# Optimization experiments

Measured on AMD Instinct MI355X. Metric: run time of the kernel, lower is better.

Reference implementation:

```python
import jax, jax.numpy as jnp
import numpy as np

N, E, G = 50000, 800000, 128
IN, HID, HEAD = 1280, 256, 4
DH = HID // HEAD
EPS = 1e-5
ATT_SCALE = 1.0 / np.sqrt(1280.0).astype(np.float32)  # hardcoded in source


def _seg_softmax(x, seg, n):
    # softmax over segments along axis 0; x: [K] or [K, H]
    m = jax.ops.segment_max(x, seg, num_segments=n)
    e = jnp.exp(x - m[seg])
    s = jax.ops.segment_sum(e, seg, num_segments=n)
    return e / s[seg]


def _bn(x, g, b):
    # eval-mode BatchNorm1d with init running stats (mean=0, var=1)
    return g * x * (1.0 / np.sqrt(1.0 + EPS)) + b


def _ln(x, g, b):
    mu = x.mean(-1, keepdims=True)
    var = ((x - mu) ** 2).mean(-1, keepdims=True)
    return g * (x - mu) / jnp.sqrt(var + EPS) + b


def setup_inputs() -> dict:
    key = jax.random.key(0)
    ks = jax.random.split(key, 40)
    rn = lambda i, shp, s=0.05: jax.random.normal(ks[i], shp, jnp.float32) * s
    inp = {
        "h": jax.random.normal(ks[0], (N, IN), jnp.float32),
        "gcn_w0": rn(1, (IN, HID)), "gcn_b0": rn(2, (HID,), 0.01),
        "gcn_w1": rn(3, (HID, HID)), "gcn_b1": rn(4, (HID,), 0.01),
        "bn_gcn0_g": 1.0 + rn(5, (HID,), 0.1), "bn_gcn0_b": rn(6, (HID,), 0.01),
        "bn_gcn1_g": 1.0 + rn(7, (HID,), 0.1), "bn_gcn1_b": rn(8, (HID,), 0.01),
        "gat_w0": rn(9, (IN, HID)), "gat_al0": rn(10, (HEAD, DH)), "gat_ar0": rn(11, (HEAD, DH)), "gat_bias0": rn(12, (HID,), 0.01),
        "gat_w1": rn(13, (HID, HID)), "gat_al1": rn(14, (HEAD, DH)), "gat_ar1": rn(15, (HEAD, DH)), "gat_bias1": rn(16, (HID,), 0.01),
        "bn_gat0_g": 1.0 + rn(17, (HID,), 0.1), "bn_gat0_b": rn(18, (HID,), 0.01),
        "bn_gat1_g": 1.0 + rn(19, (HID,), 0.1), "bn_gat1_b": rn(20, (HID,), 0.01),
        "gate_w": rn(21, (2 * HID, HID)), "gate_b": rn(22, (HID,), 0.01),
        "qw": rn(23, (HEAD, HID, HID)), "kw": rn(24, (HEAD, HID, HID)), "vw": rn(25, (HEAD, HID, HID)),
        "ct_w": rn(26, (HEAD * HID, HID)),
        "ff_w1": rn(27, (HID, 2 * HID)), "ff_b1": rn(28, (2 * HID,), 0.01),
        "ff_w2": rn(29, (2 * HID, HID)), "ff_b2": rn(30, (HID,), 0.01),
        "ln_g": 1.0 + rn(31, (HID,), 0.1), "ln_b": rn(32, (HID,), 0.01),
        "src": jax.random.randint(ks[33], (E,), 0, N, jnp.int32),
        "dst": jax.random.randint(ks[34], (E,), 0, N, jnp.int32),
        "gid": jnp.sort(jax.random.randint(ks[35], (N,), 0, G, jnp.int32)),
        "num_graphs": G,
    }
    return inp


def reference(h, gcn_w0, gcn_b0, gcn_w1, gcn_b1, bn_gcn0_g, bn_gcn0_b, bn_gcn1_g, bn_gcn1_b,
              gat_w0, gat_al0, gat_ar0, gat_bias0, gat_w1, gat_al1, gat_ar1, gat_bias1,
              bn_gat0_g, bn_gat0_b, bn_gat1_g, bn_gat1_b, gate_w, gate_b,
              qw, kw, vw, ct_w, ff_w1, ff_b1, ff_w2, ff_b2, ln_g, ln_b,
              src, dst, gid, num_graphs):
    n = h.shape[0]
    ones_e = jnp.ones(src.shape[0], h.dtype)
    # dgl.mean_nodes per graph
    cnt = jnp.clip(jax.ops.segment_sum(jnp.ones(n, h.dtype), gid, num_segments=num_graphs), 1.0)
    init_avg_h = jax.ops.segment_sum(h, gid, num_segments=num_graphs) / cnt[:, None]
    # GraphConv norm='both', degrees clamped to >=1
    deg_out = jnp.clip(jax.ops.segment_sum(ones_e, src, num_segments=n), 1.0)
    deg_in = jnp.clip(jax.ops.segment_sum(ones_e, dst, num_segments=n), 1.0)
    ns, nd = deg_out ** -0.5, deg_in ** -0.5

    def gcn(x, w, b):
        m = (x * ns[:, None]) @ w  # [N, HID]
        return jax.ops.segment_sum(m[src], dst, num_segments=n) * nd[:, None] + b

    hg = jax.nn.relu(_bn(gcn(h, gcn_w0, gcn_b0), bn_gcn0_g, bn_gcn0_b))
    hg = jax.nn.relu(_bn(gcn(hg, gcn_w1, gcn_b1), bn_gcn1_g, bn_gcn1_b)) + hg

    def gat(x, w, al, ar, b):
        f = (x @ w).reshape(n, HEAD, DH)
        el = (f * al).sum(-1)  # [N, HEAD]
        er = (f * ar).sum(-1)
        e = jax.nn.leaky_relu(el[src] + er[dst], 0.2)  # [E, HEAD]
        alpha = _seg_softmax(e, dst, n)  # edge softmax over incoming edges
        out = jax.ops.segment_sum(alpha[:, :, None] * f[src], dst, num_segments=n)
        return out.reshape(n, HID) + b

    ha = jax.nn.elu(_bn(gat(h, gat_w0, gat_al0, gat_ar0, gat_bias0), bn_gat0_g, bn_gat0_b))
    ha = jax.nn.elu(_bn(gat(ha, gat_w1, gat_al1, gat_ar1, gat_bias1), bn_gat1_g, bn_gat1_b)) + ha

    gate = jax.nn.sigmoid(jnp.concatenate([hg, ha], axis=1) @ gate_w + gate_b)
    x = gate * hg + (1.0 - gate) * ha  # residue_h

    # transformer_block: per-graph node softmax attention
    q = jnp.einsum('nd,hde->nhe', x, qw)
    k = jnp.einsum('nd,hde->nhe', x, kw)
    v = jnp.einsum('nd,hde->nhe', x, vw)
    att = (q * k).sum(-1) * ATT_SCALE  # [N, HEAD]
    alpha = _seg_softmax(att, gid, num_graphs)  # dgl.softmax_nodes per head
    mo = (v * alpha[:, :, None]).reshape(n, HEAD * HID) @ ct_w
    x1 = _ln(mo + x, ln_g, ln_b)
    x2 = _ln(jax.nn.relu(x1 @ ff_w1 + ff_b1) @ ff_w2 + ff_b2 + x1, ln_g, ln_b)

    readout = jax.ops.segment_sum(x2, gid, num_segments=num_graphs)
    return readout, init_avg_h
```

## Files before the change

### kernel.cpp

```cpp
#include <hip/hip_runtime.h>

#define NN 50000
#define NE 800000
#define NG 128
#define DIN 1280
#define HIDDEN 256
#define BNS 0.9999950000374997f
#define ATT_SCALE 0.027950849718747373f
#define LN_EPS 1e-5f

typedef __attribute__((ext_vector_type(8))) short short8;
typedef __attribute__((ext_vector_type(4))) float floatx4;

__device__ __forceinline__ float b2f(unsigned short u) {
  return __uint_as_float(((unsigned int)u) << 16);
}
__device__ __forceinline__ unsigned short f2b(float f) {
  unsigned int x = __float_as_uint(f);
  x += 0x7fffu + ((x >> 16) & 1u);
  return (unsigned short)(x >> 16);
}

__device__ __forceinline__ void tr_dev(const float* __restrict__ src,
                                       unsigned short* __restrict__ dst,
                                       int K, int Nc, int bi) {
  int idx = bi * 256 + threadIdx.x;
  if (idx >= K * Nc) return;
  int n = idx / K, k = idx % K;
  dst[idx] = f2b(src[(size_t)k * Nc + n]);
}

__global__ void prep_all_k(const float* __restrict__ gcn_w0, const float* __restrict__ gat_w0,
                           const float* __restrict__ gcn_w1, const float* __restrict__ gat_w1,
                           const float* __restrict__ gate_w, const float* __restrict__ ff_w1,
                           const float* __restrict__ ff_w2, const float* __restrict__ qw,
                           const float* __restrict__ kw, const float* __restrict__ vw,
                           const float* __restrict__ ctw,
                           unsigned short* __restrict__ w01t, unsigned short* __restrict__ w1t,
                           unsigned short* __restrict__ w1gt, unsigned short* __restrict__ gatewt,
                           unsigned short* __restrict__ ffw1t, unsigned short* __restrict__ ffw2t,
                           unsigned short* __restrict__ wmvt, unsigned short* __restrict__ w2t) {
  int b = blockIdx.x;
  if (b < 1280) { tr_dev(gcn_w0, w01t, 1280, 256, b); return; }
  if (b < 2560) { tr_dev(gat_w0, w01t + 256 * 1280, 1280, 256, b - 1280); return; }
  if (b < 2816) { tr_dev(gcn_w1, w1t, 256, 256, b - 2560); return; }
  if (b < 3072) { tr_dev(gat_w1, w1gt, 256, 256, b - 2816); return; }
  if (b < 3584) { tr_dev(gate_w, gatewt, 512, 256, b - 3072); return; }
  if (b < 4096) { tr_dev(ff_w1, ffw1t, 256, 512, b - 3584); return; }
  if (b < 4608) { tr_dev(ff_w2, ffw2t, 512, 256, b - 4096); return; }
  if (b < 5632) {
    int col = b - 4608;
    int d = threadIdx.x;
    int hh = col >> 8, dp = col & 255;
    const float* qr = qw + ((size_t)hh * 256 + d) * 256;
    const float* kr = kw + ((size_t)hh * 256 + dp) * 256;
    float s = 0.f;
    for (int e = 0; e < 256; e += 4) {
      float4 a = *(const float4*)(qr + e);
      float4 bb = *(const float4*)(kr + e);
      s += a.x * bb.x + a.y * bb.y + a.z * bb.z + a.w * bb.w;
    }
    wmvt[(size_t)col * 256 + d] = f2b(s);
    return;
  }
  {
    int bb = b - 5632;
    int c = threadIdx.x;
    int hh = bb >> 8, d = bb & 255;
    const float* vr = vw + ((size_t)hh * 256 + d) * 256;
    float s = 0.f;
    for (int e = 0; e < 256; ++e)
      s += vr[e] * ctw[(size_t)(hh * 256 + e) * 256 + c];
    w2t[(size_t)c * 1024 + bb] = f2b(s);
  }
}

__global__ void cvt_avg_k(const float* __restrict__ h, const int* __restrict__ gid,
                          unsigned short* __restrict__ h_bf, float* __restrict__ out1) {
  int row0 = blockIdx.x * 50;
  int tid = threadIdx.x;
  float4 acc = {0.f, 0.f, 0.f, 0.f};
  int cur_g = gid[row0];
  int c4 = tid * 4;
  for (int r = 0; r < 50; ++r) {
    int row = row0 + r;
    int g = gid[row];
    if (g != cur_g) {
      atomicAdd(&out1[(size_t)cur_g * DIN + c4 + 0], acc.x);
      atomicAdd(&out1[(size_t)cur_g * DIN + c4 + 1], acc.y);
      atomicAdd(&out1[(size_t)cur_g * DIN + c4 + 2], acc.z);
      atomicAdd(&out1[(size_t)cur_g * DIN + c4 + 3], acc.w);
      acc = {0.f, 0.f, 0.f, 0.f};
      cur_g = g;
    }
    float4 v = *(const float4*)(h + (size_t)row * DIN + c4);
    acc.x += v.x; acc.y += v.y; acc.z += v.z; acc.w += v.w;
    ushort4 o;
    o.x = f2b(v.x); o.y = f2b(v.y); o.z = f2b(v.z); o.w = f2b(v.w);
    *(ushort4*)(h_bf + (size_t)row * DIN + c4) = o;
  }
  atomicAdd(&out1[(size_t)cur_g * DIN + c4 + 0], acc.x);
  atomicAdd(&out1[(size_t)cur_g * DIN + c4 + 1], acc.y);
  atomicAdd(&out1[(size_t)cur_g * DIN + c4 + 2], acc.z);
  atomicAdd(&out1[(size_t)cur_g * DIN + c4 + 3], acc.w);
}

__global__ void div_avg_k(const int* __restrict__ start, float* __restrict__ out1) {
  int idx = blockIdx.x * 256 + threadIdx.x;
  if (idx >= NG * DIN) return;
  int g = idx / DIN;
  float cnt = (float)(start[g + 1] - start[g]);
  if (cnt < 1.f) cnt = 1.f;
  out1[idx] /= cnt;
}

__global__ void bounds_deg_k(const int* __restrict__ gid, int* __restrict__ start,
                             const int* __restrict__ src, const int* __restrict__ dst,
                             int* __restrict__ deg_out, int* __restrict__ deg_in) {
  int i = blockIdx.x * 256 + threadIdx.x;
  if (i < NN) {
    int g = gid[i];
    if (i == 0) {
      for (int gg = 0; gg <= g; ++gg) start[gg] = 0;
    } else {
      int gp = gid[i - 1];
      for (int gg = gp + 1; gg <= g; ++gg) start[gg] = i;
    }
    if (i == NN - 1) {
      for (int gg = g + 1; gg <= NG; ++gg) start[gg] = NN;
    }
  }
  if (i < NE) {
    atomicAdd(&deg_out[src[i]], 1);
    atomicAdd(&deg_in[dst[i]], 1);
  }
}

__global__ void scan_local_k(const int* __restrict__ deg_in, const int* __restrict__ deg_out,
                             int* __restrict__ row_ptr, int* __restrict__ bsum,
                             float* __restrict__ ns, float* __restrict__ nd) {
  __shared__ int buf[256];
  int b = blockIdx.x, t = threadIdx.x;
  int i = b * 256 + t;
  int v = (i < NN) ? deg_in[i] : 0;
  buf[t] = v;
  __syncthreads();
  for (int off = 1; off < 256; off <<= 1) {
    int tv = (t >= off) ? buf[t - off] : 0;
    __syncthreads();
    buf[t] += tv;
    __syncthreads();
  }
  if (i < NN) {
    row_ptr[i] = buf[t] - v;
    int a = deg_out[i]; if (a < 1) a = 1;
    int bb = v;         if (bb < 1) bb = 1;
    ns[i] = rsqrtf((float)a);
    nd[i] = rsqrtf((float)bb);
  }
  if (t == 255) bsum[b] = buf[255];
}

__global__ void scan_bsum_k(int* __restrict__ bsum, int* __restrict__ boff, int nb,
                            int* __restrict__ row_ptr) {
  __shared__ int buf[256];
  int t = threadIdx.x;
  int v = (t < nb) ? bsum[t] : 0;
  buf[t] = v;
  __syncthreads();
  for (int off = 1; off < 256; off <<= 1) {
    int tv = (t >= off) ? buf[t - off] : 0;
    __syncthreads();
    buf[t] += tv;
    __syncthreads();
  }
  if (t < nb) boff[t] = buf[t] - v;
  if (t == 0) row_ptr[NN] = NE;
}

__global__ void scan_add_k(int* __restrict__ row_ptr, const int* __restrict__ boff) {
  int i = blockIdx.x * 256 + threadIdx.x;
  if (i >= NN) return;
  row_ptr[i] += boff[blockIdx.x];
}

__global__ void fill_csr_k(const int* __restrict__ src, const int* __restrict__ dst,
                           const int* __restrict__ row_ptr, int* __restrict__ fill,
                           int* __restrict__ csr_src, int e) {
  int i = blockIdx.x * 256 + threadIdx.x;
  if (i >= e) return;
  int d = dst[i];
  int pos = row_ptr[d] + atomicAdd(&fill[d], 1);
  csr_src[pos] = src[i];
}

template <int MODE>
__global__ __launch_bounds__(256, 2) void gemm_bf16(const unsigned short* __restrict__ A,
                                                    const unsigned short* __restrict__ Bt,
                                                    void* __restrict__ Cout,
                                                    const float* __restrict__ bias,
                                                    int M, int K, int Nc,
                                                    const unsigned short* __restrict__ xtile,
                                                    float* __restrict__ attp,
                                                    const float* __restrict__ ascale,
                                                    const float* __restrict__ al,
                                                    const float* __restrict__ ar,
                                                    float* __restrict__ elr,
                                                    int ecol0) {
  __shared__ unsigned short sbuf[32768];
  const int tid = threadIdx.x;
  const int n0 = blockIdx.x * 128;
  const int m0 = blockIdx.y * 128;
  const int w = tid >> 6;
  const int lane = tid & 63;
  const int wr = (w >> 1) * 64;
  const int wc = (w & 1) * 64;
  const int quad = lane >> 4;
  const int l15 = lane & 15;
  const int js = tid & 7;
  const int mbase = tid >> 3;
  const int wbase = w * 64;

  bool do_elr = (MODE == 8);
  const unsigned short* Ap = A;
  const unsigned short* Bp = Bt;
  unsigned short* Cp = (unsigned short*)Cout;
  if (MODE == 8 && gridDim.z == 2) {
    if (blockIdx.z == 0) {
      do_elr = false;
    } else {
      Ap += 12800000;
      Bp += 65536;
      Cp += 12800000;
    }
  }

  floatx4 acc[4][4];
#pragma unroll
  for (int i = 0; i < 4; ++i)
#pragma unroll
    for (int j = 0; j < 4; ++j) acc[i][j] = (floatx4)0.0f;

  if constexpr (MODE == 6) {
    unsigned short* lA = sbuf;
    unsigned short* lB = sbuf + 8192;
    for (int k0 = 0; k0 < K; k0 += 64) {
      __syncthreads();
#pragma unroll
      for (int it = 0; it < 4; ++it) {
        int m = it * 32 + mbase;
        int gm = m0 + m;
        if (gm >= M) gm = M - 1;
        uint4 va = *(const uint4*)(Ap + (size_t)gm * 256 + (k0 & 255) + js * 8);
        float s = ascale[(size_t)gm * 4 + (k0 >> 8)];
        unsigned short* pp = (unsigned short*)&va;
#pragma unroll
        for (int c = 0; c < 8; ++c) pp[c] = f2b(b2f(pp[c]) * s);
        *(uint4*)(lA + (size_t)(m * 8 + (js ^ (m & 7))) * 8) = va;
      }
#pragma unroll
      for (int it = 0; it < 4; ++it) {
        int c = it * 256 + wbase + lane;
        int m = c >> 3, g = c & 7;
        int gn = n0 + m;
        const unsigned short* gp = Bp + (size_t)gn * K + k0 + (g ^ (m & 7)) * 8;
        __builtin_amdgcn_global_load_lds(
            (const __attribute__((address_space(1))) unsigned int*)gp,
            (__attribute__((address_space(3))) unsigned int*)(lB + (size_t)(it * 256 + wbase) * 8),
            16, 0, 0);
      }
      __syncthreads();
#pragma unroll
      for (int ks = 0; ks < 2; ++ks) {
        int kb = ks * 4 + quad;
        short8 af[4], bfr[4];
#pragma unroll
        for (int ri = 0; ri < 4; ++ri) {
          int r = wr + ri * 16 + l15;
          af[ri] = *(const short8*)(lA + (size_t)(r * 8 + (kb ^ (r & 7))) * 8);
        }
#pragma unroll
        for (int ci = 0; ci < 4; ++ci) {
          int c = wc + ci * 16 + l15;
          bfr[ci] = *(const short8*)(lB + (size_t)(c * 8 + (kb ^ (c & 7))) * 8);
        }
#pragma unroll
        for (int ri = 0; ri < 4; ++ri)
#pragma unroll
          for (int ci = 0; ci < 4; ++ci)
            acc[ri][ci] = __builtin_amdgcn_mfma_f32_16x16x32_bf16(af[ri], bfr[ci], acc[ri][ci], 0, 0, 0);
      }
    }
    __syncthreads();
  } else {
    const int nt = K >> 6;
    auto stage = [&](int b, int k0) {
      unsigned short* lA = sbuf + b * 16384;
      unsigned short* lB = lA + 8192;
#pragma unroll
      for (int it = 0; it < 4; ++it) {
        int c = it * 256 + wbase + lane;
        int m = c >> 3, g = c & 7;
        int gm = m0 + m;
        if (gm >= M) gm = M - 1;
        const unsigned short* gp = Ap + (size_t)gm * K + k0 + (g ^ (m & 7)) * 8;
        __builtin_amdgcn_global_load_lds(
            (const __attribute__((address_space(1))) unsigned int*)gp,
            (__attribute__((address_space(3))) unsigned int*)(lA + (size_t)(it * 256 + wbase) * 8),
            16, 0, 0);
      }
#pragma unroll
      for (int it = 0; it < 4; ++it) {
        int c = it * 256 + wbase + lane;
        int m = c >> 3, g = c & 7;
        int gn = n0 + m;
        const unsigned short* gp = Bp + (size_t)gn * K + k0 + (g ^ (m & 7)) * 8;
        __builtin_amdgcn_global_load_lds(
            (const __attribute__((address_space(1))) unsigned int*)gp,
            (__attribute__((address_space(3))) unsigned int*)(lB + (size_t)(it * 256 + wbase) * 8),
            16, 0, 0);
      }
    };
    stage(0, 0);
    __syncthreads();
    for (int t = 0; t < nt; ++t) {
      int cur = t & 1;
      if (t + 1 < nt) stage(cur ^ 1, (t + 1) * 64);
      unsigned short* lA = sbuf + cur * 16384;
      unsigned short* lB = lA + 8192;
#pragma unroll
      for (int ks = 0; ks < 2; ++ks) {
        int kb = ks * 4 + quad;
        short8 af[4], bfr[4];
#pragma unroll
        for (int ri = 0; ri < 4; ++ri) {
          int r = wr + ri * 16 + l15;
          af[ri] = *(const short8*)(lA + (size_t)(r * 8 + (kb ^ (r & 7))) * 8);
        }
#pragma unroll
        for (int ci = 0; ci < 4; ++ci) {
          int c = wc + ci * 16 + l15;
          bfr[ci] = *(const short8*)(lB + (size_t)(c * 8 + (kb ^ (c & 7))) * 8);
        }
#pragma unroll
        for (int ri = 0; ri < 4; ++ri)
#pragma unroll
          for (int ci = 0; ci < 4; ++ci)
            acc[ri][ci] = __builtin_amdgcn_mfma_f32_16x16x32_bf16(af[ri], bfr[ci], acc[ri][ci], 0, 0, 0);
      }
      __syncthreads();
    }
  }

  if (MODE == 4) {
    int cb = n0 & 255;
#pragma unroll
    for (int it2 = 0; it2 < 8; ++it2) {
      int linear = it2 * 256 + tid;
      int rr = linear >> 4;
      int c8 = (linear & 15) * 8;
      int gr = m0 + rr;
      if (gr >= M) gr = M - 1;
      *(uint4*)(sbuf + rr * 128 + c8) = *(const uint4*)(xtile + (size_t)gr * 256 + cb + c8);
    }
    __syncthreads();
    int head = n0 >> 8;
#pragma unroll
    for (int ri = 0; ri < 4; ++ri) {
      int lrow = wr + ri * 16 + quad * 4;
#pragma unroll
      for (int r = 0; r < 4; ++r) {
        float p = 0.f;
#pragma unroll
        for (int ci = 0; ci < 4; ++ci)
          p += acc[ri][ci][r] * b2f(sbuf[(lrow + r) * 128 + wc + ci * 16 + l15]);
        p += __shfl_xor(p, 1);
        p += __shfl_xor(p, 2);
        p += __shfl_xor(p, 4);
        p += __shfl_xor(p, 8);
        if (l15 == 0) {
          int grow = m0 + lrow + r;
          if (grow < M) atomicAdd(&attp[(size_t)grow * 4 + head], p * ATT_SCALE);
        }
      }
    }
    return;
  }

  if (MODE == 7) {
#pragma unroll
    for (int ri = 0; ri < 4; ++ri) {
      int row = m0 + wr + ri * 16 + quad * 4;
#pragma unroll
      for (int ci = 0; ci < 4; ++ci) {
        int col = n0 + wc + ci * 16 + l15;
        float bv = bias[col];
#pragma unroll
        for (int r = 0; r < 4; ++r) {
          if (row + r < M) {
            float g = 1.f / (1.f + expf(-(acc[ri][ci][r] + bv)));
            float hg = b2f(xtile[(size_t)(row + r) * 512 + col]);
            float ha = b2f(xtile[(size_t)(row + r) * 512 + 256 + col]);
            Cp[(size_t)(row + r) * Nc + col] = f2b(g * hg + (1.f - g) * ha);
          }
        }
      }
    }
    return;
  }

  if (MODE == 8 && do_elr && n0 >= ecol0) {
    int head = (n0 - ecol0 + wc) >> 6;
#pragma unroll
    for (int ri = 0; ri < 4; ++ri) {
      int lrow = wr + ri * 16 + quad * 4;
#pragma unroll
      for (int r = 0; r < 4; ++r) {
        float pl = 0.f, pr = 0.f;
#pragma unroll
        for (int ci = 0; ci < 4; ++ci) {
          float fv = acc[ri][ci][r];
          pl += fv * al[head * 64 + ci * 16 + l15];
          pr += fv * ar[head * 64 + ci * 16 + l15];
        }
        pl += __shfl_xor(pl, 1); pl += __shfl_xor(pl, 2);
        pl += __shfl_xor(pl, 4); pl += __shfl_xor(pl, 8);
        pr += __shfl_xor(pr, 1); pr += __shfl_xor(pr, 2);
        pr += __shfl_xor(pr, 4); pr += __shfl_xor(pr, 8);
        if (l15 == 0) {
          int grow = m0 + lrow + r;
          if (grow < M) {
            elr[(size_t)grow * 8 + head] = pl;
            elr[(size_t)grow * 8 + 4 + head] = pr;
          }
        }
      }
    }
  }

#pragma unroll
  for (int ri = 0; ri < 4; ++ri) {
    int row = m0 + wr + ri * 16 + quad * 4;
#pragma unroll
    for (int ci = 0; ci < 4; ++ci) {
      int col = n0 + wc + ci * 16 + l15;
      float bv = (MODE == 2) ? bias[col] : 0.f;
#pragma unroll
      for (int r = 0; r < 4; ++r) {
        if (row + r < M) {
          float v = acc[ri][ci][r];
          if (MODE == 2) { v += bv; v = fmaxf(v, 0.f); }
          if (MODE == 1)
            ((float*)Cout)[(size_t)(row + r) * Nc + col] = v;
          else
            Cp[(size_t)(row + r) * Nc + col] = f2b(v);
        }
      }
    }
  }
}

__global__ void gcn_agg_k(const unsigned short* __restrict__ m, int ldm,
                          const int* __restrict__ row_ptr, const int* __restrict__ csr_src,
                          const float* __restrict__ ns, const float* __restrict__ nd,
                          const float* __restrict__ bias,
                          const float* __restrict__ bng, const float* __restrict__ bnb,
                          const unsigned short* __restrict__ resid, int ldr,
                          unsigned short* __restrict__ out, int ldo) {
  int node = blockIdx.x * 4 + (threadIdx.x >> 6);
  if (node >= NN) return;
  int lane = threadIdx.x & 63;
  int s = row_ptr[node], e = row_ptr[node + 1];
  int eidx = lane & 15;
  float a0 = 0, a1 = 0, a2 = 0, a3 = 0;
  for (int i0 = s; i0 < e; i0 += 16) {
    int n16 = e - i0; if (n16 > 16) n16 = 16;
    int u_mine = 0; float w_mine = 0.f;
    if (eidx < n16) {
      u_mine = csr_src[i0 + eidx];
      w_mine = ns[u_mine];
    }
    for (int e2 = 0; e2 < n16; ++e2) {
      int sl = (lane & 48) | e2;
      int u = __shfl(u_mine, sl);
      float w = __shfl(w_mine, sl);
      ushort4 v = *(const ushort4*)(m + (size_t)u * ldm + lane * 4);
      a0 += w * b2f(v.x); a1 += w * b2f(v.y); a2 += w * b2f(v.z); a3 += w * b2f(v.w);
    }
  }
  float ndv = nd[node];
  int col = lane * 4;
  float vals[4] = {a0, a1, a2, a3};
  ushort4 o;
#pragma unroll
  for (int c = 0; c < 4; ++c) {
    float v = vals[c] * ndv + bias[col + c];
    v = bng[col + c] * v * BNS + bnb[col + c];
    v = fmaxf(v, 0.f);
    if (resid) v += b2f(resid[(size_t)node * ldr + col + c]);
    ((unsigned short*)&o)[c] = f2b(v);
  }
  *(ushort4*)(out + (size_t)node * ldo + col) = o;
}

__global__ void gat_agg_k(const unsigned short* __restrict__ f, int ldf,
                          const int* __restrict__ row_ptr, const int* __restrict__ csr_src,
                          const float* __restrict__ elr,
                          const float* __restrict__ bias,
                          const float* __restrict__ bng, const float* __restrict__ bnb,
                          const unsigned short* __restrict__ resid, int ldr,
                          unsigned short* __restrict__ out, int ldo) {
  int node = blockIdx.x * 4 + (threadIdx.x >> 6);
  if (node >= NN) return;
  int lane = threadIdx.x & 63;
  int s = row_ptr[node], e = row_ptr[node + 1];
  float4 er = *(const float4*)(elr + (size_t)node * 8 + 4);
  float m0 = -1e30f, m1 = -1e30f, m2 = -1e30f, m3 = -1e30f;
  for (int i = s + lane; i < e; i += 64) {
    int u = csr_src[i];
    float4 el = *(const float4*)(elr + (size_t)u * 8);
    float t;
    t = el.x + er.x; t = t > 0.f ? t : 0.2f * t; m0 = fmaxf(m0, t);
    t = el.y + er.y; t = t > 0.f ? t : 0.2f * t; m1 = fmaxf(m1, t);
    t = el.z + er.z; t = t > 0.f ? t : 0.2f * t; m2 = fmaxf(m2, t);
    t = el.w + er.w; t = t > 0.f ? t : 0.2f * t; m3 = fmaxf(m3, t);
  }
#pragma unroll
  for (int off = 1; off < 64; off <<= 1) {
    m0 = fmaxf(m0, __shfl_xor(m0, off));
    m1 = fmaxf(m1, __shfl_xor(m1, off));
    m2 = fmaxf(m2, __shfl_xor(m2, off));
    m3 = fmaxf(m3, __shfl_xor(m3, off));
  }
  float s0 = 0, s1 = 0, s2 = 0, s3 = 0;
  for (int i = s + lane; i < e; i += 64) {
    int u = csr_src[i];
    float4 el = *(const float4*)(elr + (size_t)u * 8);
    float t;
    t = el.x + er.x; t = t > 0.f ? t : 0.2f * t; s0 += expf(t - m0);
    t = el.y + er.y; t = t > 0.f ? t : 0.2f * t; s1 += expf(t - m1);
    t = el.z + er.z; t = t > 0.f ? t : 0.2f * t; s2 += expf(t - m2);
    t = el.w + er.w; t = t > 0.f ? t : 0.2f * t; s3 += expf(t - m3);
  }
#pragma unroll
  for (int off = 1; off < 64; off <<= 1) {
    s0 += __shfl_xor(s0, off);
    s1 += __shfl_xor(s1, off);
    s2 += __shfl_xor(s2, off);
    s3 += __shfl_xor(s3, off);
  }
  int head = lane >> 4;
  float erh = head == 0 ? er.x : head == 1 ? er.y : head == 2 ? er.z : er.w;
  float mh = head == 0 ? m0 : head == 1 ? m1 : head == 2 ? m2 : m3;
  float sh = head == 0 ? s0 : head == 1 ? s1 : head == 2 ? s2 : s3;
  float inv_sh = (sh > 0.f) ? 1.f / sh : 0.f;
  int eidx = lane & 15;
  float a0 = 0, a1 = 0, a2 = 0, a3 = 0;
  for (int i0 = s; i0 < e; i0 += 16) {
    int n16 = e - i0; if (n16 > 16) n16 = 16;
    int u_mine = 0; float w_mine = 0.f;
    if (eidx < n16) {
      u_mine = csr_src[i0 + eidx];
      float el = elr[(size_t)u_mine * 8 + head];
      float t = el + erh;
      t = t > 0.f ? t : 0.2f * t;
      w_mine = expf(t - mh) * inv_sh;
    }
    for (int e2 = 0; e2 < n16; ++e2) {
      int sl = (lane & 48) | e2;
      int u = __shfl(u_mine, sl);
      float wgt = __shfl(w_mine, sl);
      ushort4 v = *(const ushort4*)(f + (size_t)u * ldf + lane * 4);
      a0 += wgt * b2f(v.x); a1 += wgt * b2f(v.y); a2 += wgt * b2f(v.z); a3 += wgt * b2f(v.w);
    }
  }
  int col = lane * 4;
  float vals[4] = {a0, a1, a2, a3};
  ushort4 o;
#pragma unroll
  for (int c = 0; c < 4; ++c) {
    float v = vals[c] + bias[col + c];
    v = bng[col + c] * v * BNS + bnb[col + c];
    v = (v > 0.f) ? v : (expf(v) - 1.f);
    if (resid) v += b2f(resid[(size_t)node * ldr + col + c]);
    ((unsigned short*)&o)[c] = f2b(v);
  }
  *(ushort4*)(out + (size_t)node * ldo + col) = o;
}

__global__ void gsoftmax_k(const float* __restrict__ att, const int* __restrict__ start,
                           float* __restrict__ alpha) {
  int g = blockIdx.x;
  int s = start[g], e = start[g + 1];
  int tid = threadIdx.x;
  __shared__ float red[256];
  __shared__ float mh[4], sh[4];
  float lm[4] = {-1e30f, -1e30f, -1e30f, -1e30f};
  for (int i = s + tid; i < e; i += 256) {
    float4 a = *(const float4*)(att + (size_t)i * 4);
    lm[0] = fmaxf(lm[0], a.x); lm[1] = fmaxf(lm[1], a.y);
    lm[2] = fmaxf(lm[2], a.z); lm[3] = fmaxf(lm[3], a.w);
  }
#pragma unroll
  for (int h = 0; h < 4; ++h) {
    red[tid] = lm[h]; __syncthreads();
    for (int off = 128; off > 0; off >>= 1) {
      if (tid < off) red[tid] = fmaxf(red[tid], red[tid + off]);
      __syncthreads();
    }
    if (tid == 0) mh[h] = red[0];
    __syncthreads();
  }
  float ls[4] = {0, 0, 0, 0};
  for (int i = s + tid; i < e; i += 256) {
    float4 a = *(const float4*)(att + (size_t)i * 4);
    ls[0] += expf(a.x - mh[0]); ls[1] += expf(a.y - mh[1]);
    ls[2] += expf(a.z - mh[2]); ls[3] += expf(a.w - mh[3]);
  }
#pragma unroll
  for (int h = 0; h < 4; ++h) {
    red[tid] = ls[h]; __syncthreads();
    for (int off = 128; off > 0; off >>= 1) {
      if (tid < off) red[tid] += red[tid + off];
      __syncthreads();
    }
    if (tid == 0) sh[h] = red[0];
    __syncthreads();
  }
  for (int i = s + tid; i < e; i += 256) {
    float4 a = *(const float4*)(att + (size_t)i * 4);
    float4 o;
    o.x = expf(a.x - mh[0]) / sh[0];
    o.y = expf(a.y - mh[1]) / sh[1];
    o.z = expf(a.z - mh[2]) / sh[2];
    o.w = expf(a.w - mh[3]) / sh[3];
    *(float4*)(alpha + (size_t)i * 4) = o;
  }
}

__global__ void ln1_k(const unsigned short* __restrict__ mo, const unsigned short* __restrict__ x,
                      const float* __restrict__ g, const float* __restrict__ b,
                      unsigned short* __restrict__ x1) {
  int node = blockIdx.x * 4 + (threadIdx.x >> 6);
  if (node >= NN) return;
  int lane = threadIdx.x & 63;
  int c = lane * 4;
  ushort4 a = *(const ushort4*)(mo + (size_t)node * HIDDEN + c);
  ushort4 xx = *(const ushort4*)(x + (size_t)node * HIDDEN + c);
  float v0 = b2f(a.x) + b2f(xx.x), v1 = b2f(a.y) + b2f(xx.y);
  float v2 = b2f(a.z) + b2f(xx.z), v3 = b2f(a.w) + b2f(xx.w);
  float sm = v0 + v1 + v2 + v3;
#pragma unroll
  for (int off = 1; off < 64; off <<= 1) sm += __shfl_xor(sm, off);
  float mu = sm * (1.f / 256.f);
  float d0 = v0 - mu, d1 = v1 - mu, d2 = v2 - mu, d3 = v3 - mu;
  float sq = d0 * d0 + d1 * d1 + d2 * d2 + d3 * d3;
#pragma unroll
  for (int off = 1; off < 64; off <<= 1) sq += __shfl_xor(sq, off);
  float inv = rsqrtf(sq * (1.f / 256.f) + LN_EPS);
  ushort4 ob;
  ob.x = f2b(g[c + 0] * d0 * inv + b[c + 0]);
  ob.y = f2b(g[c + 1] * d1 * inv + b[c + 1]);
  ob.z = f2b(g[c + 2] * d2 * inv + b[c + 2]);
  ob.w = f2b(g[c + 3] * d3 * inv + b[c + 3]);
  *(ushort4*)(x1 + (size_t)node * HIDDEN + c) = ob;
}

__global__ void ln2_k(const unsigned short* __restrict__ ff2o, const float* __restrict__ ffb2,
                      const unsigned short* __restrict__ x1,
                      const float* __restrict__ g, const float* __restrict__ b,
                      unsigned short* __restrict__ x2) {
  int node = blockIdx.x * 4 + (threadIdx.x >> 6);
  if (node >= NN) return;
  int lane = threadIdx.x & 63;
  int c = lane * 4;
  ushort4 a = *(const ushort4*)(ff2o + (size_t)node * HIDDEN + c);
  ushort4 xx = *(const ushort4*)(x1 + (size_t)node * HIDDEN + c);
  float v0 = b2f(a.x) + ffb2[c + 0] + b2f(xx.x), v1 = b2f(a.y) + ffb2[c + 1] + b2f(xx.y);
  float v2 = b2f(a.z) + ffb2[c + 2] + b2f(xx.z), v3 = b2f(a.w) + ffb2[c + 3] + b2f(xx.w);
  float sm = v0 + v1 + v2 + v3;
#pragma unroll
  for (int off = 1; off < 64; off <<= 1) sm += __shfl_xor(sm, off);
  float mu = sm * (1.f / 256.f);
  float d0 = v0 - mu, d1 = v1 - mu, d2 = v2 - mu, d3 = v3 - mu;
  float sq = d0 * d0 + d1 * d1 + d2 * d2 + d3 * d3;
#pragma unroll
  for (int off = 1; off < 64; off <<= 1) sq += __shfl_xor(sq, off);
  float inv = rsqrtf(sq * (1.f / 256.f) + LN_EPS);
  ushort4 ob;
  ob.x = f2b(g[c + 0] * d0 * inv + b[c + 0]);
  ob.y = f2b(g[c + 1] * d1 * inv + b[c + 1]);
  ob.z = f2b(g[c + 2] * d2 * inv + b[c + 2]);
  ob.w = f2b(g[c + 3] * d3 * inv + b[c + 3]);
  *(ushort4*)(x2 + (size_t)node * HIDDEN + c) = ob;
}

__global__ void readout_k(const unsigned short* __restrict__ x2, const int* __restrict__ start,
                          float* __restrict__ out0) {
  int g = blockIdx.x;
  int c = threadIdx.x;
  float acc = 0.f;
  for (int i = start[g]; i < start[g + 1]; ++i) acc += b2f(x2[(size_t)i * HIDDEN + c]);
  out0[(size_t)g * HIDDEN + c] = acc;
}

static const size_t OFF_BUFA   = 0;
static const size_t OFF_C01    = 128000000;
static const size_t OFF_HG0    = 179200000;
static const size_t OFF_HA0    = 204800000;
static const size_t OFF_M1     = 230400000;
static const size_t OFF_F1     = 256000000;
static const size_t OFF_XCAT   = 281600000;
static const size_t OFF_XB     = 358400000;
static const size_t OFF_MO     = 384000000;
static const size_t OFF_X1     = 409600000;
static const size_t OFF_ATT    = 435200000;
static const size_t OFF_ALPHA  = OFF_ATT + 800000;
static const size_t OFF_ELR0   = OFF_ALPHA + 800000;
static const size_t OFF_ELR1   = OFF_ELR0 + 1600000;
static const size_t OFF_START  = OFF_ELR1 + 1600000;
static const size_t OFF_DEGO   = OFF_START + 1024;
static const size_t OFF_DEGI   = OFF_DEGO + 200704;
static const size_t OFF_FILL   = OFF_DEGI + 200704;
static const size_t OFF_NS     = OFF_FILL + 200704;
static const size_t OFF_ND     = OFF_NS + 200704;
static const size_t OFF_ROWP   = OFF_ND + 200704;
static const size_t OFF_BSUM   = OFF_ROWP + 200704;
static const size_t OFF_BOFF   = OFF_BSUM + 1024;
static const size_t OFF_CSRS   = OFF_BOFF + 1024;
static const size_t OFF_W01T   = OFF_CSRS + 3200000;
static const size_t OFF_W1T    = OFF_W01T + 1310720;
static const size_t OFF_W1GT   = OFF_W1T + 131072;
static const size_t OFF_GATEWT = OFF_W1GT + 131072;
static const size_t OFF_WMVT   = OFF_GATEWT + 262144;
static const size_t OFF_CTWT   = OFF_WMVT + 1048576;
static const size_t OFF_FFW1T  = OFF_CTWT + 524288;
static const size_t OFF_FFW2T  = OFF_FFW1T + 262144;
static const size_t WS_NEED    = OFF_FFW2T + 262144;

extern "C" void kernel_launch(void* const* d_in, const int* in_sizes, int n_in,
                              void* d_out, int out_size, void* d_ws, size_t ws_size,
                              hipStream_t stream) {
  if (ws_size < WS_NEED) return;

  const float* h       = (const float*)d_in[0];
  const float* gcn_w0  = (const float*)d_in[1];
  const float* gcn_b0  = (const float*)d_in[2];
  const float* gcn_w1  = (const float*)d_in[3];
  const float* gcn_b1  = (const float*)d_in[4];
  const float* bn_gcn0_g = (const float*)d_in[5];
  const float* bn_gcn0_b = (const float*)d_in[6];
  const float* bn_gcn1_g = (const float*)d_in[7];
  const float* bn_gcn1_b = (const float*)d_in[8];
  const float* gat_w0  = (const float*)d_in[9];
  const float* gat_al0 = (const float*)d_in[10];
  const float* gat_ar0 = (const float*)d_in[11];
  const float* gat_bias0 = (const float*)d_in[12];
  const float* gat_w1  = (const float*)d_in[13];
  const float* gat_al1 = (const float*)d_in[14];
  const float* gat_ar1 = (const float*)d_in[15];
  const float* gat_bias1 = (const float*)d_in[16];
  const float* bn_gat0_g = (const float*)d_in[17];
  const float* bn_gat0_b = (const float*)d_in[18];
  const float* bn_gat1_g = (const float*)d_in[19];
  const float* bn_gat1_b = (const float*)d_in[20];
  const float* gate_w  = (const float*)d_in[21];
  const float* gate_b  = (const float*)d_in[22];
  const float* qw      = (const float*)d_in[23];
  const float* kw      = (const float*)d_in[24];
  const float* vw      = (const float*)d_in[25];
  const float* ct_w    = (const float*)d_in[26];
  const float* ff_w1   = (const float*)d_in[27];
  const float* ff_b1   = (const float*)d_in[28];
  const float* ff_w2   = (const float*)d_in[29];
  const float* ff_b2   = (const float*)d_in[30];
  const float* ln_g    = (const float*)d_in[31];
  const float* ln_b    = (const float*)d_in[32];
  const int* srcv = (const int*)d_in[33];
  const int* dstv = (const int*)d_in[34];
  const int* gid  = (const int*)d_in[35];

  char* ws = (char*)d_ws;
  unsigned short* h_bf = (unsigned short*)(ws + OFF_BUFA);
  unsigned short* ff1o = (unsigned short*)(ws + OFF_BUFA);
  unsigned short* ff2o = (unsigned short*)(ws + OFF_BUFA + 51200000);
  unsigned short* x2   = (unsigned short*)(ws + OFF_BUFA + 76800000);
  unsigned short* c01  = (unsigned short*)(ws + OFF_C01);
  unsigned short* hg0  = (unsigned short*)(ws + OFF_HG0);
  unsigned short* ha0  = (unsigned short*)(ws + OFF_HA0);
  unsigned short* m1   = (unsigned short*)(ws + OFF_M1);
  unsigned short* f1   = (unsigned short*)(ws + OFF_F1);
  unsigned short* xcat = (unsigned short*)(ws + OFF_XCAT);
  unsigned short* xb   = (unsigned short*)(ws + OFF_XB);
  unsigned short* mo   = (unsigned short*)(ws + OFF_MO);
  unsigned short* x1   = (unsigned short*)(ws + OFF_X1);
  float* att           = (float*)(ws + OFF_ATT);
  float* alpha         = (float*)(ws + OFF_ALPHA);
  float* elr0          = (float*)(ws + OFF_ELR0);
  float* elr1          = (float*)(ws + OFF_ELR1);
  int* start   = (int*)(ws + OFF_START);
  int* deg_out = (int*)(ws + OFF_DEGO);
  int* deg_in  = (int*)(ws + OFF_DEGI);
  int* fill    = (int*)(ws + OFF_FILL);
  float* ns    = (float*)(ws + OFF_NS);
  float* nd    = (float*)(ws + OFF_ND);
  int* row_ptr = (int*)(ws + OFF_ROWP);
  int* bsum    = (int*)(ws + OFF_BSUM);
  int* boff    = (int*)(ws + OFF_BOFF);
  int* csr_src = (int*)(ws + OFF_CSRS);
  unsigned short* w01t   = (unsigned short*)(ws + OFF_W01T);
  unsigned short* w1t    = (unsigned short*)(ws + OFF_W1T);
  unsigned short* w1gt   = (unsigned short*)(ws + OFF_W1GT);
  unsigned short* gatewt = (unsigned short*)(ws + OFF_GATEWT);
  unsigned short* wmvt   = (unsigned short*)(ws + OFF_WMVT);
  unsigned short* w2t    = (unsigned short*)(ws + OFF_CTWT);
  unsigned short* ffw1t  = (unsigned short*)(ws + OFF_FFW1T);
  unsigned short* ffw2t  = (unsigned short*)(ws + OFF_FFW2T);

  float* out0 = (float*)d_out;
  float* out1 = out0 + NG * HIDDEN;

  hipMemsetAsync(deg_out, 0, 3 * 200704, stream);
  hipMemsetAsync(out1, 0, NG * DIN * 4, stream);
  hipMemsetAsync(att, 0, NN * 4 * 4, stream);

  prep_all_k<<<6656, 256, 0, stream>>>(gcn_w0, gat_w0, gcn_w1, gat_w1, gate_w, ff_w1, ff_w2,
                                       qw, kw, vw, ct_w,
                                       w01t, w1t, w1gt, gatewt, ffw1t, ffw2t, wmvt, w2t);

  bounds_deg_k<<<(NE + 255) / 256, 256, 0, stream>>>(gid, start, srcv, dstv, deg_out, deg_in);
  const int NB_SCAN = (NN + 255) / 256;
  scan_local_k<<<NB_SCAN, 256, 0, stream>>>(deg_in, deg_out, row_ptr, bsum, ns, nd);
  scan_bsum_k<<<1, 256, 0, stream>>>(bsum, boff, NB_SCAN, row_ptr);
  scan_add_k<<<NB_SCAN, 256, 0, stream>>>(row_ptr, boff);
  fill_csr_k<<<(NE + 255) / 256, 256, 0, stream>>>(srcv, dstv, row_ptr, fill, csr_src, NE);

  cvt_avg_k<<<NN / 50, 320, 0, stream>>>(h, gid, h_bf, out1);
  div_avg_k<<<(NG * DIN + 255) / 256, 256, 0, stream>>>(start, out1);

  const int MB = (NN + 127) / 128;
  gemm_bf16<8><<<dim3(4, MB), 256, 0, stream>>>(h_bf, w01t, c01, nullptr, NN, 1280, 512,
                                                nullptr, nullptr, nullptr,
                                                gat_al0, gat_ar0, elr0, 256);
  gcn_agg_k<<<NN / 4, 256, 0, stream>>>(c01, 512, row_ptr, csr_src, ns, nd,
                                        gcn_b0, bn_gcn0_g, bn_gcn0_b, nullptr, 0, hg0, 256);
  gat_agg_k<<<NN / 4, 256, 0, stream>>>(c01 + 256, 512, row_ptr, csr_src, elr0,
                                        gat_bias0, bn_gat0_g, bn_gat0_b, nullptr, 0, ha0, 256);
  gemm_bf16<8><<<dim3(2, MB, 2), 256, 0, stream>>>(hg0, w1t, m1, nullptr, NN, 256, 256,
                                                   nullptr, nullptr, nullptr,
                                                   gat_al1, gat_ar1, elr1, 0);
  gcn_agg_k<<<NN / 4, 256, 0, stream>>>(m1, 256, row_ptr, csr_src, ns, nd,
                                        gcn_b1, bn_gcn1_g, bn_gcn1_b, hg0, 256, xcat, 512);
  gat_agg_k<<<NN / 4, 256, 0, stream>>>(f1, 256, row_ptr, csr_src, elr1,
                                        gat_bias1, bn_gat1_g, bn_gat1_b, ha0, 256, xcat + 256, 512);
  gemm_bf16<7><<<dim3(2, MB), 256, 0, stream>>>(xcat, gatewt, xb, gate_b, NN, 512, 256,
                                                xcat, nullptr, nullptr,
                                                nullptr, nullptr, nullptr, 0);
  gemm_bf16<4><<<dim3(8, MB), 256, 0, stream>>>(xb, wmvt, nullptr, nullptr, NN, 256, 1024,
                                                xb, att, nullptr,
                                                nullptr, nullptr, nullptr, 0);
  gsoftmax_k<<<NG, 256, 0, stream>>>(att, start, alpha);
  gemm_bf16<6><<<dim3(2, MB), 256, 0, stream>>>(xb, w2t, mo, nullptr, NN, 1024, 256,
                                                nullptr, nullptr, alpha,
                                                nullptr, nullptr, nullptr, 0);
  ln1_k<<<NN / 4, 256, 0, stream>>>(mo, xb, ln_g, ln_b, x1);
  gemm_bf16<2><<<dim3(4, MB), 256, 0, stream>>>(x1, ffw1t, ff1o, ff_b1, NN, 256, 512,
                                                nullptr, nullptr, nullptr,
                                                nullptr, nullptr, nullptr, 0);
  gemm_bf16<0><<<dim3(2, MB), 256, 0, stream>>>(ff1o, ffw2t, ff2o, nullptr, NN, 512, 256,
                                                nullptr, nullptr, nullptr,
                                                nullptr, nullptr, nullptr, 0);
  ln2_k<<<NN / 4, 256, 0, stream>>>(ff2o, ff_b2, x1, ln_g, ln_b, x2);
  readout_k<<<NG, 256, 0, stream>>>(x2, start, out0);
}
```

Measured before the change: 1.576 ms.

## Fuse GCN and GAT neighbor aggregation kernels and remap GEMM blocks per XCD

Merges the separate GCN and GAT CSR aggregation kernels into one kernel. The combined kernel walks each node's edge list once and reads both halves of an interleaved 512-wide feature row, which removes duplicate CSR and index traffic and two launches per layer. The second-layer GEMM now writes its two z-slices into one interleaved buffer through a column offset so the fused kernel can read both. It also adds a workgroup-ID swizzle so consecutive tiles land on the same XCD, aiming for better L2 reuse. In exchange the fused kernel uses more registers per thread.

```diff
diff --git a/kernel.cpp b/kernel.cpp
--- a/kernel.cpp
+++ b/kernel.cpp
@@ -209,8 +209,14 @@
                                                     int ecol0) {
   __shared__ unsigned short sbuf[32768];
   const int tid = threadIdx.x;
-  const int n0 = blockIdx.x * 128;
-  const int m0 = blockIdx.y * 128;
+  const int gx = gridDim.x;
+  const int nwg = gx * gridDim.y;
+  const int orig = blockIdx.y * gx + blockIdx.x;
+  const int xcd = orig & 7;
+  const int q = nwg >> 3, r = nwg & 7;
+  const int wg = (xcd < r ? xcd * (q + 1) : r * (q + 1) + (xcd - r) * q) + (orig >> 3);
+  const int n0 = (wg % gx) * 128;
+  const int m0 = (wg / gx) * 128;
   const int w = tid >> 6;
   const int lane = tid & 63;
   const int wr = (w >> 1) * 64;
@@ -222,6 +228,7 @@
   const int wbase = w * 64;
 
   bool do_elr = (MODE == 8);
+  int cz = 0;
   const unsigned short* Ap = A;
   const unsigned short* Bp = Bt;
   unsigned short* Cp = (unsigned short*)Cout;
@@ -231,7 +238,7 @@
     } else {
       Ap += 12800000;
       Bp += 65536;
-      Cp += 12800000;
+      cz = 256;
     }
   }
 
@@ -276,8 +283,8 @@
         short8 af[4], bfr[4];
 #pragma unroll
         for (int ri = 0; ri < 4; ++ri) {
-          int r = wr + ri * 16 + l15;
-          af[ri] = *(const short8*)(lA + (size_t)(r * 8 + (kb ^ (r & 7))) * 8);
+          int rr = wr + ri * 16 + l15;
+          af[ri] = *(const short8*)(lA + (size_t)(rr * 8 + (kb ^ (rr & 7))) * 8);
         }
 #pragma unroll
         for (int ci = 0; ci < 4; ++ci) {
@@ -334,8 +341,8 @@
         short8 af[4], bfr[4];
 #pragma unroll
         for (int ri = 0; ri < 4; ++ri) {
-          int r = wr + ri * 16 + l15;
-          af[ri] = *(const short8*)(lA + (size_t)(r * 8 + (kb ^ (r & 7))) * 8);
+          int rr = wr + ri * 16 + l15;
+          af[ri] = *(const short8*)(lA + (size_t)(rr * 8 + (kb ^ (rr & 7))) * 8);
         }
 #pragma unroll
         for (int ci = 0; ci < 4; ++ci) {
@@ -369,17 +376,17 @@
     for (int ri = 0; ri < 4; ++ri) {
       int lrow = wr + ri * 16 + quad * 4;
 #pragma unroll
-      for (int r = 0; r < 4; ++r) {
+      for (int r2 = 0; r2 < 4; ++r2) {
         float p = 0.f;
 #pragma unroll
         for (int ci = 0; ci < 4; ++ci)
-          p += acc[ri][ci][r] * b2f(sbuf[(lrow + r) * 128 + wc + ci * 16 + l15]);
+          p += acc[ri][ci][r2] * b2f(sbuf[(lrow + r2) * 128 + wc + ci * 16 + l15]);
         p += __shfl_xor(p, 1);
         p += __shfl_xor(p, 2);
         p += __shfl_xor(p, 4);
         p += __shfl_xor(p, 8);
         if (l15 == 0) {
-          int grow = m0 + lrow + r;
+          int grow = m0 + lrow + r2;
           if (grow < M) atomicAdd(&attp[(size_t)grow * 4 + head], p * ATT_SCALE);
         }
       }
@@ -396,12 +403,12 @@
         int col = n0 + wc + ci * 16 + l15;
         float bv = bias[col];
 #pragma unroll
-        for (int r = 0; r < 4; ++r) {
-          if (row + r < M) {
-            float g = 1.f / (1.f + expf(-(acc[ri][ci][r] + bv)));
-            float hg = b2f(xtile[(size_t)(row + r) * 512 + col]);
-            float ha = b2f(xtile[(size_t)(row + r) * 512 + 256 + col]);
-            Cp[(size_t)(row + r) * Nc + col] = f2b(g * hg + (1.f - g) * ha);
+        for (int r2 = 0; r2 < 4; ++r2) {
+          if (row + r2 < M) {
+            float g = 1.f / (1.f + expf(-(acc[ri][ci][r2] + bv)));
+            float hg = b2f(xtile[(size_t)(row + r2) * 512 + col]);
+            float ha = b2f(xtile[(size_t)(row + r2) * 512 + 256 + col]);
+            Cp[(size_t)(row + r2) * Nc + col] = f2b(g * hg + (1.f - g) * ha);
           }
         }
       }
@@ -415,11 +422,11 @@
     for (int ri = 0; ri < 4; ++ri) {
       int lrow = wr + ri * 16 + quad * 4;
 #pragma unroll
-      for (int r = 0; r < 4; ++r) {
+      for (int r2 = 0; r2 < 4; ++r2) {
         float pl = 0.f, pr = 0.f;
 #pragma unroll
         for (int ci = 0; ci < 4; ++ci) {
-          float fv = acc[ri][ci][r];
+          float fv = acc[ri][ci][r2];
           pl += fv * al[head * 64 + ci * 16 + l15];
           pr += fv * ar[head * 64 + ci * 16 + l15];
         }
@@ -428,7 +435,7 @@
         pr += __shfl_xor(pr, 1); pr += __shfl_xor(pr, 2);
         pr += __shfl_xor(pr, 4); pr += __shfl_xor(pr, 8);
         if (l15 == 0) {
-          int grow = m0 + lrow + r;
+          int grow = m0 + lrow + r2;
           if (grow < M) {
             elr[(size_t)grow * 8 + head] = pl;
             elr[(size_t)grow * 8 + 4 + head] = pr;
@@ -446,70 +453,32 @@
       int col = n0 + wc + ci * 16 + l15;
       float bv = (MODE == 2) ? bias[col] : 0.f;
 #pragma unroll
-      for (int r = 0; r < 4; ++r) {
-        if (row + r < M) {
-          float v = acc[ri][ci][r];
+      for (int r2 = 0; r2 < 4; ++r2) {
+        if (row + r2 < M) {
+          float v = acc[ri][ci][r2];
           if (MODE == 2) { v += bv; v = fmaxf(v, 0.f); }
           if (MODE == 1)
-            ((float*)Cout)[(size_t)(row + r) * Nc + col] = v;
+            ((float*)Cout)[(size_t)(row + r2) * Nc + col] = v;
           else
-            Cp[(size_t)(row + r) * Nc + col] = f2b(v);
+            Cp[(size_t)(row + r2) * Nc + col + cz] = f2b(v);
         }
       }
     }
   }
 }
 
-__global__ void gcn_agg_k(const unsigned short* __restrict__ m, int ldm,
-                          const int* __restrict__ row_ptr, const int* __restrict__ csr_src,
-                          const float* __restrict__ ns, const float* __restrict__ nd,
-                          const float* __restrict__ bias,
-                          const float* __restrict__ bng, const float* __restrict__ bnb,
-                          const unsigned short* __restrict__ resid, int ldr,
-                          unsigned short* __restrict__ out, int ldo) {
-  int node = blockIdx.x * 4 + (threadIdx.x >> 6);
-  if (node >= NN) return;
-  int lane = threadIdx.x & 63;
-  int s = row_ptr[node], e = row_ptr[node + 1];
-  int eidx = lane & 15;
-  float a0 = 0, a1 = 0, a2 = 0, a3 = 0;
-  for (int i0 = s; i0 < e; i0 += 16) {
-    int n16 = e - i0; if (n16 > 16) n16 = 16;
-    int u_mine = 0; float w_mine = 0.f;
-    if (eidx < n16) {
-      u_mine = csr_src[i0 + eidx];
-      w_mine = ns[u_mine];
-    }
-    for (int e2 = 0; e2 < n16; ++e2) {
-      int sl = (lane & 48) | e2;
-      int u = __shfl(u_mine, sl);
-      float w = __shfl(w_mine, sl);
-      ushort4 v = *(const ushort4*)(m + (size_t)u * ldm + lane * 4);
-      a0 += w * b2f(v.x); a1 += w * b2f(v.y); a2 += w * b2f(v.z); a3 += w * b2f(v.w);
-    }
-  }
-  float ndv = nd[node];
-  int col = lane * 4;
-  float vals[4] = {a0, a1, a2, a3};
-  ushort4 o;
-#pragma unroll
-  for (int c = 0; c < 4; ++c) {
-    float v = vals[c] * ndv + bias[col + c];
-    v = bng[col + c] * v * BNS + bnb[col + c];
-    v = fmaxf(v, 0.f);
-    if (resid) v += b2f(resid[(size_t)node * ldr + col + c]);
-    ((unsigned short*)&o)[c] = f2b(v);
-  }
-  *(ushort4*)(out + (size_t)node * ldo + col) = o;
-}
-
-__global__ void gat_agg_k(const unsigned short* __restrict__ f, int ldf,
-                          const int* __restrict__ row_ptr, const int* __restrict__ csr_src,
-                          const float* __restrict__ elr,
-                          const float* __restrict__ bias,
-                          const float* __restrict__ bng, const float* __restrict__ bnb,
-                          const unsigned short* __restrict__ resid, int ldr,
-                          unsigned short* __restrict__ out, int ldo) {
+__global__ void agg_both_k(const unsigned short* __restrict__ mf,
+                           const int* __restrict__ row_ptr, const int* __restrict__ csr_src,
+                           const float* __restrict__ ns, const float* __restrict__ nd,
+                           const float* __restrict__ elr,
+                           const float* __restrict__ gcn_b, const float* __restrict__ bng_g,
+                           const float* __restrict__ bnb_g,
+                           const float* __restrict__ gat_b, const float* __restrict__ bng_a,
+                           const float* __restrict__ bnb_a,
+                           const unsigned short* __restrict__ resid_g,
+                           const unsigned short* __restrict__ resid_a,
+                           unsigned short* __restrict__ out_g, int ldo_g,
+                           unsigned short* __restrict__ out_a, int ldo_a) {
   int node = blockIdx.x * 4 + (threadIdx.x >> 6);
   if (node >= NN) return;
   int lane = threadIdx.x & 63;
@@ -555,37 +524,49 @@
   float sh = head == 0 ? s0 : head == 1 ? s1 : head == 2 ? s2 : s3;
   float inv_sh = (sh > 0.f) ? 1.f / sh : 0.f;
   int eidx = lane & 15;
+  float g0 = 0, g1 = 0, g2 = 0, g3 = 0;
   float a0 = 0, a1 = 0, a2 = 0, a3 = 0;
   for (int i0 = s; i0 < e; i0 += 16) {
     int n16 = e - i0; if (n16 > 16) n16 = 16;
-    int u_mine = 0; float w_mine = 0.f;
+    int u_mine = 0; float wg_mine = 0.f, wa_mine = 0.f;
     if (eidx < n16) {
       u_mine = csr_src[i0 + eidx];
-      float el = elr[(size_t)u_mine * 8 + head];
-      float t = el + erh;
+      wg_mine = ns[u_mine];
+      float t = elr[(size_t)u_mine * 8 + head] + erh;
       t = t > 0.f ? t : 0.2f * t;
-      w_mine = expf(t - mh) * inv_sh;
+      wa_mine = expf(t - mh) * inv_sh;
     }
     for (int e2 = 0; e2 < n16; ++e2) {
       int sl = (lane & 48) | e2;
       int u = __shfl(u_mine, sl);
-      float wgt = __shfl(w_mine, sl);
-      ushort4 v = *(const ushort4*)(f + (size_t)u * ldf + lane * 4);
-      a0 += wgt * b2f(v.x); a1 += wgt * b2f(v.y); a2 += wgt * b2f(v.z); a3 += wgt * b2f(v.w);
-    }
-  }
+      float wgv = __shfl(wg_mine, sl);
+      float wav = __shfl(wa_mine, sl);
+      ushort4 vg = *(const ushort4*)(mf + (size_t)u * 512 + lane * 4);
+      ushort4 va = *(const ushort4*)(mf + (size_t)u * 512 + 256 + lane * 4);
+      g0 += wgv * b2f(vg.x); g1 += wgv * b2f(vg.y); g2 += wgv * b2f(vg.z); g3 += wgv * b2f(vg.w);
+      a0 += wav * b2f(va.x); a1 += wav * b2f(va.y); a2 += wav * b2f(va.z); a3 += wav * b2f(va.w);
+    }
+  }
+  float ndv = nd[node];
   int col = lane * 4;
-  float vals[4] = {a0, a1, a2, a3};
-  ushort4 o;
+  float gvals[4] = {g0, g1, g2, g3};
+  float avals[4] = {a0, a1, a2, a3};
+  ushort4 og, oa;
 #pragma unroll
   for (int c = 0; c < 4; ++c) {
-    float v = vals[c] + bias[col + c];
-    v = bng[col + c] * v * BNS + bnb[col + c];
-    v = (v > 0.f) ? v : (expf(v) - 1.f);
-    if (resid) v += b2f(resid[(size_t)node * ldr + col + c]);
-    ((unsigned short*)&o)[c] = f2b(v);
-  }
-  *(ushort4*)(out + (size_t)node * ldo + col) = o;
+    float v = gvals[c] * ndv + gcn_b[col + c];
+    v = bng_g[col + c] * v * BNS + bnb_g[col + c];
+    v = fmaxf(v, 0.f);
+    if (resid_g) v += b2f(resid_g[(size_t)node * 256 + col + c]);
+    ((unsigned short*)&og)[c] = f2b(v);
+    float v2 = avals[c] + gat_b[col + c];
+    v2 = bng_a[col + c] * v2 * BNS + bnb_a[col + c];
+    v2 = (v2 > 0.f) ? v2 : (expf(v2) - 1.f);
+    if (resid_a) v2 += b2f(resid_a[(size_t)node * 256 + col + c]);
+    ((unsigned short*)&oa)[c] = f2b(v2);
+  }
+  *(ushort4*)(out_g + (size_t)node * ldo_g + col) = og;
+  *(ushort4*)(out_a + (size_t)node * ldo_a + col) = oa;
 }
 
 __global__ void gsoftmax_k(const float* __restrict__ att, const int* __restrict__ start,
@@ -708,8 +689,7 @@
 static const size_t OFF_C01    = 128000000;
 static const size_t OFF_HG0    = 179200000;
 static const size_t OFF_HA0    = 204800000;
-static const size_t OFF_M1     = 230400000;
-static const size_t OFF_F1     = 256000000;
+static const size_t OFF_MF     = 230400000;
 static const size_t OFF_XCAT   = 281600000;
 static const size_t OFF_XB     = 358400000;
 static const size_t OFF_MO     = 384000000;
@@ -788,8 +768,7 @@
   unsigned short* c01  = (unsigned short*)(ws + OFF_C01);
   unsigned short* hg0  = (unsigned short*)(ws + OFF_HG0);
   unsigned short* ha0  = (unsigned short*)(ws + OFF_HA0);
-  unsigned short* m1   = (unsigned short*)(ws + OFF_M1);
-  unsigned short* f1   = (unsigned short*)(ws + OFF_F1);
+  unsigned short* mf   = (unsigned short*)(ws + OFF_MF);
   unsigned short* xcat = (unsigned short*)(ws + OFF_XCAT);
   unsigned short* xb   = (unsigned short*)(ws + OFF_XB);
   unsigned short* mo   = (unsigned short*)(ws + OFF_MO);
@@ -842,17 +821,17 @@
   gemm_bf16<8><<<dim3(4, MB), 256, 0, stream>>>(h_bf, w01t, c01, nullptr, NN, 1280, 512,
                                                 nullptr, nullptr, nullptr,
                                                 gat_al0, gat_ar0, elr0, 256);
-  gcn_agg_k<<<NN / 4, 256, 0, stream>>>(c01, 512, row_ptr, csr_src, ns, nd,
-                                        gcn_b0, bn_gcn0_g, bn_gcn0_b, nullptr, 0, hg0, 256);
-  gat_agg_k<<<NN / 4, 256, 0, stream>>>(c01 + 256, 512, row_ptr, csr_src, elr0,
-                                        gat_bias0, bn_gat0_g, bn_gat0_b, nullptr, 0, ha0, 256);
-  gemm_bf16<8><<<dim3(2, MB, 2), 256, 0, stream>>>(hg0, w1t, m1, nullptr, NN, 256, 256,
+  agg_both_k<<<NN / 4, 256, 0, stream>>>(c01, row_ptr, csr_src, ns, nd, elr0,
+                                         gcn_b0, bn_gcn0_g, bn_gcn0_b,
+                                         gat_bias0, bn_gat0_g, bn_gat0_b,
+                                         nullptr, nullptr, hg0, 256, ha0, 256);
+  gemm_bf16<8><<<dim3(2, MB, 2), 256, 0, stream>>>(hg0, w1t, mf, nullptr, NN, 256, 512,
                                                    nullptr, nullptr, nullptr,
                                                    gat_al1, gat_ar1, elr1, 0);
-  gcn_agg_k<<<NN / 4, 256, 0, stream>>>(m1, 256, row_ptr, csr_src, ns, nd,
-                                        gcn_b1, bn_gcn1_g, bn_gcn1_b, hg0, 256, xcat, 512);
-  gat_agg_k<<<NN / 4, 256, 0, stream>>>(f1, 256, row_ptr, csr_src, elr1,
-                                        gat_bias1, bn_gat1_g, bn_gat1_b, ha0, 256, xcat + 256, 512);
+  agg_both_k<<<NN / 4, 256, 0, stream>>>(mf, row_ptr, csr_src, ns, nd, elr1,
+                                         gcn_b1, bn_gcn1_g, bn_gcn1_b,
+                                         gat_bias1, bn_gat1_g, bn_gat1_b,
+                                         hg0, ha0, xcat, 512, xcat + 256, 512);
   gemm_bf16<7><<<dim3(2, MB), 256, 0, stream>>>(xcat, gatewt, xb, gate_b, NN, 512, 256,
                                                 xcat, nullptr, nullptr,
                                                 nullptr, nullptr, nullptr, 0);
```

Result: faster. 1.539 ms (-2.3%).
